# Kernel tuning notes

Measured on AMD Instinct MI355X. Metric: run time of the kernel, lower is better.

The kernel has to match this reference:

```python
import jax, jax.numpy as jnp
import numpy as np

B, T, F = 4096, 60, 30
H, HD, LAT = 256, 100, 256
ACQ_VOCAB = [(50, 16), (10, 8), (5, 4)]
SEQ_VOCAB = [(30, 8), (12, 4), (31, 4)]
DIN = F + 28 + 16  # 74 = seq_n_features + emb_acq_sum + emb_seq_sum
EPS = 1e-5


def setup_inputs() -> dict:
    key = jax.random.key(0)
    ks = iter(jax.random.split(key, 64))

    def nrm(shape, s=0.05):
        return jax.random.normal(next(ks), shape, jnp.float32) * s

    inp = {}
    inp["seq"] = jax.random.normal(next(ks), (B, T, F), jnp.float32)
    inp["seq_len"] = jnp.sort(jax.random.randint(next(ks), (B,), 1, T + 1))[::-1]  # descending (pack_padded)
    inp["ymd"] = jnp.stack([jax.random.randint(next(ks), (B, T), 0, c) for c, _ in SEQ_VOCAB], axis=-1)
    inp["acq"] = jnp.stack([jax.random.randint(next(ks), (B,), 0, c) for c, _ in ACQ_VOCAB], axis=-1)
    inp["macro_pred"] = jax.random.normal(next(ks), (B, 12, 14), jnp.float32)
    inp["z_noise"] = jax.random.normal(next(ks), (B, LAT), jnp.float32)  # reparam noise, fixed for determinism
    for i, (c, d) in enumerate(ACQ_VOCAB):
        inp[f"E_acq{i}"] = nrm((c, d), 1.0)
    for i, (c, d) in enumerate(SEQ_VOCAB):
        inp[f"E_seq{i}"] = nrm((c, d), 1.0)
    for tag in ("f", "b"):  # bidirectional LSTM, 1 layer
        inp[f"Wih_{tag}"] = nrm((4 * H, DIN))
        inp[f"Whh_{tag}"] = nrm((4 * H, H))
        inp[f"bih_{tag}"] = nrm((4 * H,))
        inp[f"bhh_{tag}"] = nrm((4 * H,))
    inp["W_lat"] = nrm((2 * LAT, H)); inp["b_lat"] = nrm((2 * LAT,))
    inp["Wih1"] = nrm((4 * HD, LAT + 9 + 14)); inp["Whh1"] = nrm((4 * HD, HD))
    inp["bih1"] = nrm((4 * HD,)); inp["bhh1"] = nrm((4 * HD,))
    inp["Wih2"] = nrm((4 * HD, HD)); inp["Whh2"] = nrm((4 * HD, HD))
    inp["bih2"] = nrm((4 * HD,)); inp["bhh2"] = nrm((4 * HD,))
    inp["Wg1"] = nrm((25, HD)); inp["bg1"] = nrm((25,))
    inp["gamma"] = jnp.ones((25,), jnp.float32); inp["beta"] = jnp.zeros((25,), jnp.float32)
    inp["Wg2"] = nrm((9, 25)); inp["bg2"] = nrm((9,))
    return inp


def _lstm_cell(x, h, c, Wih, Whh, bih, bhh):
    g = x @ Wih.T + h @ Whh.T + (bih + bhh)
    i, f, gg, o = jnp.split(g, 4, axis=-1)  # torch gate order i,f,g,o
    c = jax.nn.sigmoid(f) * c + jax.nn.sigmoid(i) * jnp.tanh(gg)
    h = jax.nn.sigmoid(o) * jnp.tanh(c)
    return h, c


def _masked_lstm(xs_tm, lens, Wih, Whh, bih, bhh):
    """xs_tm: [T,B,D] time-major. Returns hidden at each sequence's final valid step."""
    h0 = jnp.zeros((xs_tm.shape[1], Whh.shape[1]), xs_tm.dtype)

    def step(carry, inp):
        h, c = carry
        x, t = inp
        hn, cn = _lstm_cell(x, h, c, Wih, Whh, bih, bhh)
        m = (t < lens)[:, None]
        return (jnp.where(m, hn, h), jnp.where(m, cn, c)), None

    (h, _), _ = jax.lax.scan(step, (h0, h0), (xs_tm, jnp.arange(xs_tm.shape[0])))
    return h


def reference(seq, seq_len, ymd, acq, macro_pred, z_noise,
              E_acq0, E_acq1, E_acq2, E_seq0, E_seq1, E_seq2,
              Wih_f, Whh_f, bih_f, bhh_f, Wih_b, Whh_b, bih_b, bhh_b,
              W_lat, b_lat, Wih1, Whh1, bih1, bhh1, Wih2, Whh2, bih2, bhh2,
              Wg1, bg1, gamma, beta, Wg2, bg2):
    Bn, Tn = seq.shape[0], seq.shape[1]
    ea = jnp.concatenate([E_acq0[acq[:, 0]], E_acq1[acq[:, 1]], E_acq2[acq[:, 2]]], axis=1)
    ea = jnp.broadcast_to(ea[:, None, :], (Bn, Tn, ea.shape[1]))
    ey = jnp.concatenate([E_seq0[ymd[:, :, 0]], E_seq1[ymd[:, :, 1]], E_seq2[ymd[:, :, 2]]], axis=2)
    s = jnp.concatenate([seq, ea, ey], axis=2)  # [B,T,74]

    # bidirectional LSTM over valid lengths (pack_padded semantics)
    h_f = _masked_lstm(jnp.swapaxes(s, 0, 1), seq_len, Wih_f, Whh_f, bih_f, bhh_f)
    idx = jnp.clip(seq_len[:, None] - 1 - jnp.arange(Tn)[None, :], 0, Tn - 1)  # per-seq reversed valid indices
    s_rev = jnp.take_along_axis(s, idx[:, :, None], axis=1)
    h_b = _masked_lstm(jnp.swapaxes(s_rev, 0, 1), seq_len, Wih_b, Whh_b, bih_b, bhh_b)

    lat = (h_f + h_b) @ W_lat.T + b_lat  # [B, 2*LAT]
    mu_z, logv = lat[:, :LAT], lat[:, LAT:]
    z = mu_z + jnp.sqrt(jnp.exp(logv)) * z_noise

    dlq0 = jnp.take_along_axis(seq, (seq_len - 1)[:, None, None], axis=1)[:, 0, -9:]  # [B,9]
    h0 = jnp.zeros((Bn, HD), seq.dtype)

    def dec_step(carry, mp_t):
        h1, c1, h2, c2, dlq = carry
        decinp = jnp.concatenate([z, dlq, mp_t], axis=1)  # [B, LAT+9+14]
        h1, c1 = _lstm_cell(decinp, h1, c1, Wih1, Whh1, bih1, bhh1)
        h2, c2 = _lstm_cell(h1, h2, c2, Wih2, Whh2, bih2, bhh2)  # dropout = identity (eval)
        x = jax.nn.relu(h2 @ Wg1.T + bg1)
        mu = x.mean(axis=0)
        var = ((x - mu) ** 2).mean(axis=0)  # train-mode BN, biased var
        x = gamma * (x - mu) * jax.lax.rsqrt(var + EPS) + beta
        dlq = x @ Wg2.T + bg2
        return (h1, c1, h2, c2, dlq), dlq

    _, outs = jax.lax.scan(dec_step, (h0, h0, h0, h0, dlq0), jnp.swapaxes(macro_pred, 0, 1))
    return jnp.transpose(outs, (1, 2, 0))  # [B, 9, 12] (torch.stack(out, 2))
```

## Files before the change

kernel.cpp:

```cpp
#include <hip/hip_runtime.h>
#include <math.h>

#define B_SZ   4096
#define T_SZ   60
#define F_SZ   30
#define H_ENC  256
#define HD_DEC 100
#define LATD   256
#define KM     352
#define KMP    360
#define NKK    11
#define DEC_IN 279
#define DTAIL  24

enum {
  OFF_PWM_F = 0,
  OFF_PWM_B = OFF_PWM_F + 180224,
  OFF_BEN_F = OFF_PWM_B + 180224,
  OFF_BEN_B = OFF_BEN_F + 1024,
  OFF_PLAT  = OFF_BEN_B + 1024,
  OFF_P1I   = OFF_PLAT + 256*256*2,
  OFF_P1H   = OFF_P1I + 280*100*4,
  OFF_P2I   = OFF_P1H + 100*100*4,
  OFF_P2H   = OFF_P2I + 100*100*4,
  OFF_WG1T  = OFF_P2H + 100*100*4,
  OFF_BE1   = OFF_WG1T + 100*25,
  OFF_BE2   = OFF_BE1 + 400,
  OFF_HF    = OFF_BE2 + 400,
  OFF_HB    = OFF_HF + B_SZ*H_ENC,
  OFF_Z     = OFF_HB + B_SZ*H_ENC,
  OFF_H1    = OFF_Z + B_SZ*LATD,
  OFF_C1    = OFF_H1 + B_SZ*HD_DEC,
  OFF_H2    = OFF_C1 + B_SZ*HD_DEC,
  OFF_C2    = OFF_H2 + B_SZ*HD_DEC,
  OFF_DLQ   = OFF_C2 + B_SZ*HD_DEC,
  OFF_XBUF  = OFF_DLQ + B_SZ*9,
  OFF_MU    = OFF_XBUF + B_SZ*25,
  OFF_RSTD  = OFF_MU + 25,
  OFF_ZW1   = OFF_RSTD + 25,
  WS_FLOATS = OFF_ZW1 + B_SZ*400
};

typedef __attribute__((ext_vector_type(8))) short short8v;
typedef __attribute__((ext_vector_type(4))) float f32x4;

__device__ __forceinline__ float sigf(float x) { return 1.0f / (1.0f + expf(-x)); }

__device__ __forceinline__ unsigned short f2bf(float f) {
  union { float f; unsigned int u; } v; v.f = f;
  unsigned int u = v.u + 0x7fffu + ((v.u >> 16) & 1u);
  return (unsigned short)(u >> 16);
}
__device__ __forceinline__ float bf2f(unsigned short s) {
  union { unsigned int u; float f; } v; v.u = ((unsigned int)s) << 16;
  return v.f;
}

struct PJob { const float* a; const float* b; float* dst; int p0, p1, p2, p3, mode; };
struct PrepArgs { PJob j[12]; };

__device__ __forceinline__ float enc_wv(const float* wih, const float* whh, int k, int u, int g) {
  if (k < 74)  return wih[(g * 256 + u) * 74 + k];
  if (k < 76)  return 0.0f;
  if (k < 332) return whh[(g * 256 + u) * 256 + (k - 76)];
  return 0.0f;
}

__global__ __launch_bounds__(256) void prep_kernel(PrepArgs pa) {
  int gtid = blockIdx.x * blockDim.x + threadIdx.x;
  int stride = gridDim.x * blockDim.x;
  for (int jj = 0; jj < 12; ++jj) {
    PJob jb = pa.j[jj];
    if (jb.mode == 1) {
      for (int i = gtid; i < jb.p0; i += stride) jb.dst[i] = jb.a[i] + jb.b[i];
    } else if (jb.mode == 0) {
      int total = jb.p2 * jb.p0;
      for (int i = gtid; i < total; i += stride) {
        int k = i / jb.p0, u = i - k * jb.p0;
        float* d = jb.dst + (size_t)i * jb.p3;
        for (int g = 0; g < jb.p3; ++g)
          d[g] = (k < jb.p1) ? jb.a[(g * jb.p0 + u) * jb.p1 + k] : 0.0f;
      }
    } else if (jb.mode == 4) {
      int total = NKK * 64 * 64;
      for (int i = gtid; i < total; i += stride) {
        int kk = i / 4096, rem = i - kk * 4096;
        int ntg = rem >> 6, l = rem & 63;
        int n = ntg * 16 + (l & 15);
        int u = n >> 2, g = n & 3;
        int kb = kk * 32 + (l >> 4) * 8;
        unsigned int* d = (unsigned int*)jb.dst + (size_t)i * 4;
        for (int wd = 0; wd < 4; ++wd) {
          float lo = enc_wv(jb.a, jb.b, kb + 2 * wd,     u, g);
          float hi = enc_wv(jb.a, jb.b, kb + 2 * wd + 1, u, g);
          d[wd] = (unsigned int)f2bf(lo) | ((unsigned int)f2bf(hi) << 16);
        }
      }
    } else {
      for (int i = gtid; i < 1024; i += stride) {
        int u = i >> 2, g = i & 3;
        jb.dst[i] = jb.a[g * 256 + u] + jb.b[g * 256 + u];
      }
    }
  }
}

#define GDOT(acc, c, w0, w1, w2, w3, xv) \
  acc = fmaf((w0).c, (xv).x, fmaf((w1).c, (xv).y, fmaf((w2).c, (xv).z, fmaf((w3).c, (xv).w, acc))))

__global__ __launch_bounds__(512) void enc_kernel(
    const float* __restrict__ seq, const int* __restrict__ seq_len,
    const int* __restrict__ ymd, const int* __restrict__ acq,
    const float* __restrict__ Ea0, const float* __restrict__ Ea1, const float* __restrict__ Ea2,
    const float* __restrict__ Es0, const float* __restrict__ Es1, const float* __restrict__ Es2,
    const unsigned short* __restrict__ PWMf, const unsigned short* __restrict__ PWMb,
    const float* __restrict__ benF, const float* __restrict__ benB,
    float* __restrict__ hf_out, float* __restrict__ hb_out)
{
  const int tid = threadIdx.x;
  const bool bwd = blockIdx.x >= 128;
  const int c = blockIdx.x & 127;
  const unsigned short* __restrict__ PWM = bwd ? PWMb : PWMf;
  const float* __restrict__ ben = bwd ? benB : benF;
  float* __restrict__ hout = bwd ? hb_out : hf_out;

  __shared__ __align__(16) unsigned short v_s[32][KMP];
  __shared__ float c_s[32][256];
  __shared__ int   len_s[32];

  for (int i = tid; i < 32 * KMP; i += 512) (&v_s[0][0])[i] = 0;
  for (int i = tid; i < 32 * 256; i += 512) (&c_s[0][0])[i] = 0.0f;
  if (tid < 32) len_s[tid] = seq_len[c + 128 * tid];
  __syncthreads();

  for (int i = tid; i < 32 * 28; i += 512) {
    int r = i / 28, d = i - r * 28;
    const int* aq = &acq[(c + 128 * r) * 3];
    float v;
    if (d < 16)      v = Ea0[aq[0] * 16 + d];
    else if (d < 24) v = Ea1[aq[1] * 8 + (d - 16)];
    else             v = Ea2[aq[2] * 4 + (d - 24)];
    v_s[r][30 + d] = f2bf(v);
  }

  const int w   = tid >> 6;
  const int l   = tid & 63;
  const int col = l & 15;
  const int qk  = l >> 4;
  const int g   = l & 3;
  const int usub = col >> 2;

  float bias_r[8];
  #pragma unroll
  for (int nt = 0; nt < 8; ++nt) bias_r[nt] = ben[128 * w + 16 * nt + col];

  __syncthreads();
  const int maxlen = len_s[0];

  for (int t = 0; t < maxlen; ++t) {
    for (int i = tid; i < 1472; i += 512) {
      if (i < 960) {
        int r = i / 30, k = i - r * 30;
        int len = len_s[r];
        int te = bwd ? max(len - 1 - t, 0) : t;
        v_s[r][k] = f2bf(seq[((size_t)(c + 128 * r) * T_SZ + te) * F_SZ + k]);
      } else {
        int ii = i - 960;
        int r = ii >> 4, d = ii & 15;
        int len = len_s[r];
        int te = bwd ? max(len - 1 - t, 0) : t;
        const int* ym = &ymd[((size_t)(c + 128 * r) * T_SZ + te) * 3];
        float v;
        if (d < 8)       v = Es0[ym[0] * 8 + d];
        else if (d < 12) v = Es1[ym[1] * 4 + (d - 8)];
        else             v = Es2[ym[2] * 4 + (d - 12)];
        v_s[r][58 + d] = f2bf(v);
      }
    }
    __syncthreads();

    f32x4 acc0[8], acc1[8];
    #pragma unroll
    for (int nt = 0; nt < 8; ++nt) {
      acc0[nt][0] = bias_r[nt]; acc0[nt][1] = bias_r[nt];
      acc0[nt][2] = bias_r[nt]; acc0[nt][3] = bias_r[nt];
      acc1[nt] = acc0[nt];
    }

    for (int kk = 0; kk < NKK; ++kk) {
      short8v a0 = *reinterpret_cast<const short8v*>(&v_s[col][32 * kk + 8 * qk]);
      short8v a1 = *reinterpret_cast<const short8v*>(&v_s[16 + col][32 * kk + 8 * qk]);
      const unsigned short* Bk = PWM + ((size_t)kk * 4096 + l) * 8;
      #pragma unroll
      for (int nt = 0; nt < 8; ++nt) {
        int ntg = 8 * w + nt;
        short8v b = *reinterpret_cast<const short8v*>(Bk + (size_t)ntg * 512);
        acc0[nt] = __builtin_amdgcn_mfma_f32_16x16x32_bf16(a0, b, acc0[nt], 0, 0, 0);
        acc1[nt] = __builtin_amdgcn_mfma_f32_16x16x32_bf16(a1, b, acc1[nt], 0, 0, 0);
      }
    }
    __syncthreads();

    #pragma unroll
    for (int rt = 0; rt < 2; ++rt) {
      #pragma unroll
      for (int nt = 0; nt < 8; ++nt) {
        int u = 32 * w + 4 * nt + usub;
        #pragma unroll
        for (int i = 0; i < 4; ++i) {
          int row = 16 * rt + qk * 4 + i;
          float val = rt == 0 ? acc0[nt][i] : acc1[nt][i];
          float act = (g == 2) ? tanhf(val) : sigf(val);
          float a1s = __shfl_xor(act, 1);
          float a2s = __shfl_xor(act, 2);
          float a3s = __shfl_xor(a1s, 2);
          if (g == 0 && t < len_s[row]) {
            float cc = c_s[row][u];
            float cn = a1s * cc + act * a2s;
            c_s[row][u] = cn;
            v_s[row][76 + u] = f2bf(a3s * tanhf(cn));
          }
        }
      }
    }
  }

  __syncthreads();
  for (int i = tid; i < 32 * 256; i += 512) {
    int r = i >> 8, u = i & 255;
    hout[(size_t)(c + 128 * r) * H_ENC + u] = bf2f(v_s[r][76 + u]);
  }
}

__global__ __launch_bounds__(256) void latent_kernel(
    const float* __restrict__ hf, const float* __restrict__ hb,
    const float2* __restrict__ Plat, const float* __restrict__ b_lat,
    const float* __restrict__ z_noise, const float* __restrict__ seq,
    const int* __restrict__ seq_len,
    float* __restrict__ z, float* __restrict__ dlq,
    float* __restrict__ h1w, float* __restrict__ c1w,
    float* __restrict__ h2w, float* __restrict__ c2w)
{
  const int tid = threadIdx.x;
  const int b0 = blockIdx.x * 16;
  __shared__ float hs[16][H_ENC];
  for (int i = tid; i < 16 * H_ENC; i += 256)
    (&hs[0][0])[i] = hf[b0 * H_ENC + i] + hb[b0 * H_ENC + i];
  __syncthreads();

  const int u = tid;
  const float bm = b_lat[u], bv = b_lat[LATD + u];
  float am[16], av[16];
  #pragma unroll
  for (int r = 0; r < 16; ++r) { am[r] = bm; av[r] = bv; }

  for (int k = 0; k < H_ENC; k += 4) {
    const float2 p0 = Plat[(k + 0) * 256 + u];
    const float2 p1 = Plat[(k + 1) * 256 + u];
    const float2 p2 = Plat[(k + 2) * 256 + u];
    const float2 p3 = Plat[(k + 3) * 256 + u];
    #pragma unroll
    for (int r = 0; r < 16; ++r) {
      const float4 hv = *reinterpret_cast<const float4*>(&hs[r][k]);
      am[r] = fmaf(p0.x, hv.x, fmaf(p1.x, hv.y, fmaf(p2.x, hv.z, fmaf(p3.x, hv.w, am[r]))));
      av[r] = fmaf(p0.y, hv.x, fmaf(p1.y, hv.y, fmaf(p2.y, hv.z, fmaf(p3.y, hv.w, av[r]))));
    }
  }
  #pragma unroll
  for (int r = 0; r < 16; ++r) {
    int b = b0 + r;
    z[b * LATD + u] = am[r] + sqrtf(expf(av[r])) * z_noise[b * LATD + u];
  }
  if (u < HD_DEC) {
    #pragma unroll
    for (int r = 0; r < 16; ++r) {
      int b = b0 + r;
      h1w[b * HD_DEC + u] = 0.0f; c1w[b * HD_DEC + u] = 0.0f;
      h2w[b * HD_DEC + u] = 0.0f; c2w[b * HD_DEC + u] = 0.0f;
    }
  }
  if (u < 9) {
    #pragma unroll
    for (int r = 0; r < 16; ++r) {
      int b = b0 + r;
      int len = seq_len[b];
      dlq[b * 9 + u] = seq[(b * T_SZ + (len - 1)) * F_SZ + 21 + u];
    }
  }
}

__global__ __launch_bounds__(256) void dec_zpre_kernel(
    const float* __restrict__ z, const float4* __restrict__ P1I,
    float* __restrict__ zw1)
{
  const int tid = threadIdx.x;
  const int b0 = blockIdx.x * 16;
  __shared__ float zs[16][LATD];
  for (int i = tid; i < 16 * LATD; i += 256)
    (&zs[0][0])[i] = z[b0 * LATD + i];
  __syncthreads();

  const int u = tid & 127;
  const int grp = tid >> 7;
  const int r0 = grp * 8;
  if (u >= HD_DEC) return;

  float a0[8], a1[8], a2[8], a3[8];
  #pragma unroll
  for (int r = 0; r < 8; ++r) { a0[r] = 0.0f; a1[r] = 0.0f; a2[r] = 0.0f; a3[r] = 0.0f; }
  for (int k = 0; k < LATD; k += 4) {
    const float4 w0 = P1I[(k + 0) * 100 + u];
    const float4 w1 = P1I[(k + 1) * 100 + u];
    const float4 w2 = P1I[(k + 2) * 100 + u];
    const float4 w3 = P1I[(k + 3) * 100 + u];
    #pragma unroll
    for (int r = 0; r < 8; ++r) {
      const float4 xv = *reinterpret_cast<const float4*>(&zs[r0 + r][k]);
      GDOT(a0[r], x, w0, w1, w2, w3, xv);
      GDOT(a1[r], y, w0, w1, w2, w3, xv);
      GDOT(a2[r], z, w0, w1, w2, w3, xv);
      GDOT(a3[r], w, w0, w1, w2, w3, xv);
    }
  }
  #pragma unroll
  for (int r = 0; r < 8; ++r) {
    int b = b0 + r0 + r;
    zw1[b * 400 + u]       = a0[r];
    zw1[b * 400 + 100 + u] = a1[r];
    zw1[b * 400 + 200 + u] = a2[r];
    zw1[b * 400 + 300 + u] = a3[r];
  }
}

__global__ __launch_bounds__(256) void dec_cell_kernel(
    const float* __restrict__ zw1, const float* __restrict__ dlq,
    const float* __restrict__ macro,
    float* __restrict__ h1w, float* __restrict__ c1w,
    float* __restrict__ h2w, float* __restrict__ c2w,
    const float4* __restrict__ P1I, const float4* __restrict__ P1H, const float* __restrict__ be1,
    const float4* __restrict__ P2I, const float4* __restrict__ P2H, const float* __restrict__ be2,
    const float* __restrict__ Wg1T, const float* __restrict__ bg1,
    float* __restrict__ xbuf, int t)
{
  const int tid = threadIdx.x;
  const int b0 = blockIdx.x * 16;
  __shared__ float di[16][DTAIL];
  __shared__ float h1s[16][HD_DEC];
  __shared__ float h2s[16][HD_DEC];

  for (int i = tid; i < 16 * DTAIL; i += 256) {
    int r = i / DTAIL, k = i - r * DTAIL;
    int b = b0 + r;
    float v;
    if (k < 9)       v = dlq[b * 9 + k];
    else if (k < 23) v = macro[(b * 12 + t) * 14 + (k - 9)];
    else             v = 0.0f;
    di[r][k] = v;
  }
  for (int i = tid; i < 16 * HD_DEC; i += 256) {
    int r = i / HD_DEC, k = i - r * HD_DEC;
    h1s[r][k] = h1w[(b0 + r) * HD_DEC + k];
    h2s[r][k] = h2w[(b0 + r) * HD_DEC + k];
  }

  const int u = tid & 127;
  const int grp = tid >> 7;
  const int r0 = grp * 8;
  const bool act = u < HD_DEC;

  float c1r[8], c2r[8];
  if (act) {
    #pragma unroll
    for (int r = 0; r < 8; ++r) {
      c1r[r] = c1w[(b0 + r0 + r) * HD_DEC + u];
      c2r[r] = c2w[(b0 + r0 + r) * HD_DEC + u];
    }
  }
  __syncthreads();

  float a0[8], a1[8], a2[8], a3[8];
  if (act) {
    const float b0g = be1[u], b1g = be1[100 + u], b2g = be1[200 + u], b3g = be1[300 + u];
    #pragma unroll
    for (int r = 0; r < 8; ++r) {
      const float* zw = &zw1[(size_t)(b0 + r0 + r) * 400];
      a0[r] = b0g + zw[u];
      a1[r] = b1g + zw[100 + u];
      a2[r] = b2g + zw[200 + u];
      a3[r] = b3g + zw[300 + u];
    }
    for (int k = 0; k < DTAIL; k += 4) {
      const int kk = LATD + k;
      const float4 w0 = P1I[(kk + 0) * 100 + u];
      const float4 w1 = P1I[(kk + 1) * 100 + u];
      const float4 w2 = P1I[(kk + 2) * 100 + u];
      const float4 w3 = P1I[(kk + 3) * 100 + u];
      #pragma unroll
      for (int r = 0; r < 8; ++r) {
        const float4 xv = *reinterpret_cast<const float4*>(&di[r0 + r][k]);
        GDOT(a0[r], x, w0, w1, w2, w3, xv);
        GDOT(a1[r], y, w0, w1, w2, w3, xv);
        GDOT(a2[r], z, w0, w1, w2, w3, xv);
        GDOT(a3[r], w, w0, w1, w2, w3, xv);
      }
    }
    for (int k = 0; k < HD_DEC; k += 4) {
      const float4 w0 = P1H[(k + 0) * 100 + u];
      const float4 w1 = P1H[(k + 1) * 100 + u];
      const float4 w2 = P1H[(k + 2) * 100 + u];
      const float4 w3 = P1H[(k + 3) * 100 + u];
      #pragma unroll
      for (int r = 0; r < 8; ++r) {
        const float4 hv = *reinterpret_cast<const float4*>(&h1s[r0 + r][k]);
        GDOT(a0[r], x, w0, w1, w2, w3, hv);
        GDOT(a1[r], y, w0, w1, w2, w3, hv);
        GDOT(a2[r], z, w0, w1, w2, w3, hv);
        GDOT(a3[r], w, w0, w1, w2, w3, hv);
      }
    }
  }
  __syncthreads();
  if (act) {
    #pragma unroll
    for (int r = 0; r < 8; ++r) {
      float ig = sigf(a0[r]), fg = sigf(a1[r]), gg = tanhf(a2[r]), og = sigf(a3[r]);
      float cn = fg * c1r[r] + ig * gg;
      float hn = og * tanhf(cn);
      int b = b0 + r0 + r;
      h1s[r0 + r][u] = hn;
      h1w[b * HD_DEC + u] = hn;
      c1w[b * HD_DEC + u] = cn;
    }
  }
  __syncthreads();

  if (act) {
    const float b0g = be2[u], b1g = be2[100 + u], b2g = be2[200 + u], b3g = be2[300 + u];
    #pragma unroll
    for (int r = 0; r < 8; ++r) { a0[r] = b0g; a1[r] = b1g; a2[r] = b2g; a3[r] = b3g; }
    for (int k = 0; k < HD_DEC; k += 4) {
      const float4 w0 = P2I[(k + 0) * 100 + u];
      const float4 w1 = P2I[(k + 1) * 100 + u];
      const float4 w2 = P2I[(k + 2) * 100 + u];
      const float4 w3 = P2I[(k + 3) * 100 + u];
      #pragma unroll
      for (int r = 0; r < 8; ++r) {
        const float4 hv = *reinterpret_cast<const float4*>(&h1s[r0 + r][k]);
        GDOT(a0[r], x, w0, w1, w2, w3, hv);
        GDOT(a1[r], y, w0, w1, w2, w3, hv);
        GDOT(a2[r], z, w0, w1, w2, w3, hv);
        GDOT(a3[r], w, w0, w1, w2, w3, hv);
      }
    }
    for (int k = 0; k < HD_DEC; k += 4) {
      const float4 w0 = P2H[(k + 0) * 100 + u];
      const float4 w1 = P2H[(k + 1) * 100 + u];
      const float4 w2 = P2H[(k + 2) * 100 + u];
      const float4 w3 = P2H[(k + 3) * 100 + u];
      #pragma unroll
      for (int r = 0; r < 8; ++r) {
        const float4 hv = *reinterpret_cast<const float4*>(&h2s[r0 + r][k]);
        GDOT(a0[r], x, w0, w1, w2, w3, hv);
        GDOT(a1[r], y, w0, w1, w2, w3, hv);
        GDOT(a2[r], z, w0, w1, w2, w3, hv);
        GDOT(a3[r], w, w0, w1, w2, w3, hv);
      }
    }
  }
  __syncthreads();
  if (act) {
    #pragma unroll
    for (int r = 0; r < 8; ++r) {
      float ig = sigf(a0[r]), fg = sigf(a1[r]), gg = tanhf(a2[r]), og = sigf(a3[r]);
      float cn = fg * c2r[r] + ig * gg;
      float hn = og * tanhf(cn);
      int b = b0 + r0 + r;
      h2s[r0 + r][u] = hn;
      h2w[b * HD_DEC + u] = hn;
      c2w[b * HD_DEC + u] = cn;
    }
  }
  __syncthreads();

  for (int p = tid; p < 16 * 25; p += 256) {
    int r = p / 25, cc = p - r * 25;
    float s = bg1[cc];
    for (int k = 0; k < HD_DEC; k += 4) {
      const float4 hv = *reinterpret_cast<const float4*>(&h2s[r][k]);
      s += hv.x * Wg1T[k * 25 + cc] + hv.y * Wg1T[(k + 1) * 25 + cc]
         + hv.z * Wg1T[(k + 2) * 25 + cc] + hv.w * Wg1T[(k + 3) * 25 + cc];
    }
    xbuf[(b0 + r) * 25 + cc] = fmaxf(s, 0.0f);
  }
}

__global__ __launch_bounds__(256) void dec_stats_kernel(
    const float* __restrict__ xbuf, float* __restrict__ muv, float* __restrict__ rstdv)
{
  const int col = blockIdx.x;
  const int tid = threadIdx.x;
  __shared__ float red[256];
  float v[16];
  float s = 0.0f;
  #pragma unroll
  for (int i = 0; i < 16; ++i) { v[i] = xbuf[(tid + 256 * i) * 25 + col]; s += v[i]; }
  red[tid] = s; __syncthreads();
  for (int off = 128; off >= 1; off >>= 1) {
    if (tid < off) red[tid] += red[tid + off];
    __syncthreads();
  }
  float mean = red[0] / (float)B_SZ;
  __syncthreads();
  float s2 = 0.0f;
  #pragma unroll
  for (int i = 0; i < 16; ++i) { float d = v[i] - mean; s2 += d * d; }
  red[tid] = s2; __syncthreads();
  for (int off = 128; off >= 1; off >>= 1) {
    if (tid < off) red[tid] += red[tid + off];
    __syncthreads();
  }
  if (tid == 0) {
    muv[col] = mean;
    rstdv[col] = rsqrtf(red[0] / (float)B_SZ + 1e-5f);
  }
}

__global__ __launch_bounds__(256) void dec_out_kernel(
    const float* __restrict__ xbuf, const float* __restrict__ muv, const float* __restrict__ rstdv,
    const float* __restrict__ gamma, const float* __restrict__ beta,
    const float* __restrict__ Wg2, const float* __restrict__ bg2,
    float* __restrict__ dlq, float* __restrict__ out, int t)
{
  int b = blockIdx.x * 256 + threadIdx.x;
  float xn[25];
  #pragma unroll
  for (int c = 0; c < 25; ++c)
    xn[c] = gamma[c] * (xbuf[b * 25 + c] - muv[c]) * rstdv[c] + beta[c];
  #pragma unroll
  for (int j = 0; j < 9; ++j) {
    float s = bg2[j];
    #pragma unroll
    for (int c = 0; c < 25; ++c) s += xn[c] * Wg2[j * 25 + c];
    dlq[b * 9 + j] = s;
    out[b * 108 + j * 12 + t] = s;
  }
}

extern "C" void kernel_launch(void* const* d_in, const int* in_sizes, int n_in,
                              void* d_out, int out_size, void* d_ws, size_t ws_size,
                              hipStream_t stream)
{
  const float* seq     = (const float*)d_in[0];
  const int*   seq_len = (const int*)  d_in[1];
  const int*   ymd     = (const int*)  d_in[2];
  const int*   acq     = (const int*)  d_in[3];
  const float* macro   = (const float*)d_in[4];
  const float* z_noise = (const float*)d_in[5];
  const float* Ea0 = (const float*)d_in[6];
  const float* Ea1 = (const float*)d_in[7];
  const float* Ea2 = (const float*)d_in[8];
  const float* Es0 = (const float*)d_in[9];
  const float* Es1 = (const float*)d_in[10];
  const float* Es2 = (const float*)d_in[11];
  const float* Wih_f = (const float*)d_in[12];
  const float* Whh_f = (const float*)d_in[13];
  const float* bih_f = (const float*)d_in[14];
  const float* bhh_f = (const float*)d_in[15];
  const float* Wih_b = (const float*)d_in[16];
  const float* Whh_b = (const float*)d_in[17];
  const float* bih_b = (const float*)d_in[18];
  const float* bhh_b = (const float*)d_in[19];
  const float* W_lat = (const float*)d_in[20];
  const float* b_lat = (const float*)d_in[21];
  const float* Wih1  = (const float*)d_in[22];
  const float* Whh1  = (const float*)d_in[23];
  const float* bih1  = (const float*)d_in[24];
  const float* bhh1  = (const float*)d_in[25];
  const float* Wih2  = (const float*)d_in[26];
  const float* Whh2  = (const float*)d_in[27];
  const float* bih2  = (const float*)d_in[28];
  const float* bhh2  = (const float*)d_in[29];
  const float* Wg1   = (const float*)d_in[30];
  const float* bg1   = (const float*)d_in[31];
  const float* gamma = (const float*)d_in[32];
  const float* beta  = (const float*)d_in[33];
  const float* Wg2   = (const float*)d_in[34];
  const float* bg2   = (const float*)d_in[35];

  float* ws  = (float*)d_ws;
  float* out = (float*)d_out;

  float* pwmF = ws + OFF_PWM_F;
  float* pwmB = ws + OFF_PWM_B;
  float* benF = ws + OFF_BEN_F;
  float* benB = ws + OFF_BEN_B;
  float* plat = ws + OFF_PLAT;
  float* p1i  = ws + OFF_P1I;
  float* p1h  = ws + OFF_P1H;
  float* p2i  = ws + OFF_P2I;
  float* p2h  = ws + OFF_P2H;
  float* wg1T = ws + OFF_WG1T;
  float* be1  = ws + OFF_BE1;
  float* be2  = ws + OFF_BE2;
  float* hf   = ws + OFF_HF;
  float* hb   = ws + OFF_HB;
  float* z    = ws + OFF_Z;
  float* h1w  = ws + OFF_H1;
  float* c1w  = ws + OFF_C1;
  float* h2w  = ws + OFF_H2;
  float* c2w  = ws + OFF_C2;
  float* dlq  = ws + OFF_DLQ;
  float* xbuf = ws + OFF_XBUF;
  float* muv  = ws + OFF_MU;
  float* rstdv= ws + OFF_RSTD;
  float* zw1  = ws + OFF_ZW1;

  PrepArgs pa;
  int ji = 0;
  auto JOB = [&](const float* a, const float* b, float* d, int p0, int p1, int p2, int p3, int m) {
    pa.j[ji].a = a; pa.j[ji].b = b; pa.j[ji].dst = d;
    pa.j[ji].p0 = p0; pa.j[ji].p1 = p1; pa.j[ji].p2 = p2; pa.j[ji].p3 = p3; pa.j[ji].mode = m; ++ji;
  };
  JOB(Wih_f, Whh_f, pwmF, 0,0,0,0, 4);
  JOB(Wih_b, Whh_b, pwmB, 0,0,0,0, 4);
  JOB(bih_f, bhh_f, benF, 0,0,0,0, 5);
  JOB(bih_b, bhh_b, benB, 0,0,0,0, 5);
  JOB(W_lat, nullptr, plat, 256, 256, 256, 2, 0);
  JOB(Wih1,  nullptr, p1i,  100, 279, 280, 4, 0);
  JOB(Whh1,  nullptr, p1h,  100, 100, 100, 4, 0);
  JOB(Wih2,  nullptr, p2i,  100, 100, 100, 4, 0);
  JOB(Whh2,  nullptr, p2h,  100, 100, 100, 4, 0);
  JOB(Wg1,   nullptr, wg1T, 25, 100, 100, 1, 0);
  JOB(bih1,  bhh1,  be1,  400, 0,0,0, 1);
  JOB(bih2,  bhh2,  be2,  400, 0,0,0, 1);

  prep_kernel<<<512, 256, 0, stream>>>(pa);

  enc_kernel<<<256, 512, 0, stream>>>(
      seq, seq_len, ymd, acq, Ea0, Ea1, Ea2, Es0, Es1, Es2,
      (const unsigned short*)pwmF, (const unsigned short*)pwmB,
      benF, benB, hf, hb);

  latent_kernel<<<256, 256, 0, stream>>>(
      hf, hb, (const float2*)plat, b_lat, z_noise, seq, seq_len,
      z, dlq, h1w, c1w, h2w, c2w);

  dec_zpre_kernel<<<256, 256, 0, stream>>>(z, (const float4*)p1i, zw1);

  for (int t = 0; t < 12; ++t) {
    dec_cell_kernel<<<256, 256, 0, stream>>>(
        zw1, dlq, macro, h1w, c1w, h2w, c2w,
        (const float4*)p1i, (const float4*)p1h, be1,
        (const float4*)p2i, (const float4*)p2h, be2, wg1T, bg1, xbuf, t);
    dec_stats_kernel<<<25, 256, 0, stream>>>(xbuf, muv, rstdv);
    dec_out_kernel<<<16, 256, 0, stream>>>(
        xbuf, muv, rstdv, gamma, beta, Wg2, bg2, dlq, out, t);
  }
}
```

Measured before the change: 3.108 ms.

## Fuse z-projection into latent kernel and BN output into next decoder cell

```diff
diff --git a/kernel.cpp b/kernel.cpp
--- a/kernel.cpp
+++ b/kernel.cpp
@@ -10,7 +10,6 @@
 #define KM     352
 #define KMP    360
 #define NKK    11
-#define DEC_IN 279
 #define DTAIL  24
 
 enum {
@@ -28,8 +27,7 @@
   OFF_BE2   = OFF_BE1 + 400,
   OFF_HF    = OFF_BE2 + 400,
   OFF_HB    = OFF_HF + B_SZ*H_ENC,
-  OFF_Z     = OFF_HB + B_SZ*H_ENC,
-  OFF_H1    = OFF_Z + B_SZ*LATD,
+  OFF_H1    = OFF_HB + B_SZ*H_ENC,
   OFF_C1    = OFF_H1 + B_SZ*HD_DEC,
   OFF_H2    = OFF_C1 + B_SZ*HD_DEC,
   OFF_C2    = OFF_H2 + B_SZ*HD_DEC,
@@ -236,8 +234,8 @@
     const float* __restrict__ hf, const float* __restrict__ hb,
     const float2* __restrict__ Plat, const float* __restrict__ b_lat,
     const float* __restrict__ z_noise, const float* __restrict__ seq,
-    const int* __restrict__ seq_len,
-    float* __restrict__ z, float* __restrict__ dlq,
+    const int* __restrict__ seq_len, const float4* __restrict__ P1I,
+    float* __restrict__ dlq, float* __restrict__ zw1,
     float* __restrict__ h1w, float* __restrict__ c1w,
     float* __restrict__ h2w, float* __restrict__ c2w)
 {
@@ -266,11 +264,6 @@
       av[r] = fmaf(p0.y, hv.x, fmaf(p1.y, hv.y, fmaf(p2.y, hv.z, fmaf(p3.y, hv.w, av[r]))));
     }
   }
-  #pragma unroll
-  for (int r = 0; r < 16; ++r) {
-    int b = b0 + r;
-    z[b * LATD + u] = am[r] + sqrtf(expf(av[r])) * z_noise[b * LATD + u];
-  }
   if (u < HD_DEC) {
     #pragma unroll
     for (int r = 0; r < 16; ++r) {
@@ -287,80 +280,96 @@
       dlq[b * 9 + u] = seq[(b * T_SZ + (len - 1)) * F_SZ + 21 + u];
     }
   }
-}
-
-__global__ __launch_bounds__(256) void dec_zpre_kernel(
-    const float* __restrict__ z, const float4* __restrict__ P1I,
-    float* __restrict__ zw1)
-{
-  const int tid = threadIdx.x;
-  const int b0 = blockIdx.x * 16;
-  __shared__ float zs[16][LATD];
-  for (int i = tid; i < 16 * LATD; i += 256)
-    (&zs[0][0])[i] = z[b0 * LATD + i];
-  __syncthreads();
-
-  const int u = tid & 127;
+  __syncthreads();
+  #pragma unroll
+  for (int r = 0; r < 16; ++r) {
+    int b = b0 + r;
+    hs[r][u] = am[r] + sqrtf(expf(av[r])) * z_noise[b * LATD + u];
+  }
+  __syncthreads();
+
+  const int uu = tid & 127;
   const int grp = tid >> 7;
   const int r0 = grp * 8;
-  if (u >= HD_DEC) return;
-
-  float a0[8], a1[8], a2[8], a3[8];
-  #pragma unroll
-  for (int r = 0; r < 8; ++r) { a0[r] = 0.0f; a1[r] = 0.0f; a2[r] = 0.0f; a3[r] = 0.0f; }
-  for (int k = 0; k < LATD; k += 4) {
-    const float4 w0 = P1I[(k + 0) * 100 + u];
-    const float4 w1 = P1I[(k + 1) * 100 + u];
-    const float4 w2 = P1I[(k + 2) * 100 + u];
-    const float4 w3 = P1I[(k + 3) * 100 + u];
+  if (uu < HD_DEC) {
+    float a0[8], a1[8], a2[8], a3[8];
+    #pragma unroll
+    for (int r = 0; r < 8; ++r) { a0[r] = 0.0f; a1[r] = 0.0f; a2[r] = 0.0f; a3[r] = 0.0f; }
+    for (int k = 0; k < LATD; k += 4) {
+      const float4 w0 = P1I[(k + 0) * 100 + uu];
+      const float4 w1 = P1I[(k + 1) * 100 + uu];
+      const float4 w2 = P1I[(k + 2) * 100 + uu];
+      const float4 w3 = P1I[(k + 3) * 100 + uu];
+      #pragma unroll
+      for (int r = 0; r < 8; ++r) {
+        const float4 xv = *reinterpret_cast<const float4*>(&hs[r0 + r][k]);
+        GDOT(a0[r], x, w0, w1, w2, w3, xv);
+        GDOT(a1[r], y, w0, w1, w2, w3, xv);
+        GDOT(a2[r], z, w0, w1, w2, w3, xv);
+        GDOT(a3[r], w, w0, w1, w2, w3, xv);
+      }
+    }
     #pragma unroll
     for (int r = 0; r < 8; ++r) {
-      const float4 xv = *reinterpret_cast<const float4*>(&zs[r0 + r][k]);
-      GDOT(a0[r], x, w0, w1, w2, w3, xv);
-      GDOT(a1[r], y, w0, w1, w2, w3, xv);
-      GDOT(a2[r], z, w0, w1, w2, w3, xv);
-      GDOT(a3[r], w, w0, w1, w2, w3, xv);
-    }
-  }
-  #pragma unroll
-  for (int r = 0; r < 8; ++r) {
-    int b = b0 + r0 + r;
-    zw1[b * 400 + u]       = a0[r];
-    zw1[b * 400 + 100 + u] = a1[r];
-    zw1[b * 400 + 200 + u] = a2[r];
-    zw1[b * 400 + 300 + u] = a3[r];
+      int b = b0 + r0 + r;
+      zw1[b * 400 + uu]       = a0[r];
+      zw1[b * 400 + 100 + uu] = a1[r];
+      zw1[b * 400 + 200 + uu] = a2[r];
+      zw1[b * 400 + 300 + uu] = a3[r];
+    }
   }
 }
 
 __global__ __launch_bounds__(256) void dec_cell_kernel(
-    const float* __restrict__ zw1, const float* __restrict__ dlq,
+    const float* __restrict__ zw1, const float* __restrict__ dlq0,
     const float* __restrict__ macro,
     float* __restrict__ h1w, float* __restrict__ c1w,
     float* __restrict__ h2w, float* __restrict__ c2w,
     const float4* __restrict__ P1I, const float4* __restrict__ P1H, const float* __restrict__ be1,
     const float4* __restrict__ P2I, const float4* __restrict__ P2H, const float* __restrict__ be2,
     const float* __restrict__ Wg1T, const float* __restrict__ bg1,
-    float* __restrict__ xbuf, int t)
+    const float* __restrict__ muv, const float* __restrict__ rstdv,
+    const float* __restrict__ gamma, const float* __restrict__ beta,
+    const float* __restrict__ Wg2, const float* __restrict__ bg2,
+    float* __restrict__ xbuf, float* __restrict__ out, int t)
 {
   const int tid = threadIdx.x;
   const int b0 = blockIdx.x * 16;
   __shared__ float di[16][DTAIL];
+  __shared__ float xns[16][25];
   __shared__ float h1s[16][HD_DEC];
   __shared__ float h2s[16][HD_DEC];
 
-  for (int i = tid; i < 16 * DTAIL; i += 256) {
-    int r = i / DTAIL, k = i - r * DTAIL;
-    int b = b0 + r;
-    float v;
-    if (k < 9)       v = dlq[b * 9 + k];
-    else if (k < 23) v = macro[(b * 12 + t) * 14 + (k - 9)];
-    else             v = 0.0f;
-    di[r][k] = v;
+  if (t > 0) {
+    for (int p = tid; p < 16 * 25; p += 256) {
+      int r = p / 25, cc = p - r * 25;
+      xns[r][cc] = gamma[cc] * (xbuf[(b0 + r) * 25 + cc] - muv[cc]) * rstdv[cc] + beta[cc];
+    }
+  } else {
+    for (int p = tid; p < 16 * 9; p += 256) {
+      int r = p / 9, j = p - r * 9;
+      di[r][j] = dlq0[(b0 + r) * 9 + j];
+    }
+  }
+  for (int i = tid; i < 16 * 15; i += 256) {
+    int r = i / 15, k = i - r * 15;
+    di[r][9 + k] = (k < 14) ? macro[((size_t)(b0 + r) * 12 + t) * 14 + k] : 0.0f;
   }
   for (int i = tid; i < 16 * HD_DEC; i += 256) {
     int r = i / HD_DEC, k = i - r * HD_DEC;
     h1s[r][k] = h1w[(b0 + r) * HD_DEC + k];
     h2s[r][k] = h2w[(b0 + r) * HD_DEC + k];
+  }
+  __syncthreads();
+  if (t > 0) {
+    for (int p = tid; p < 16 * 9; p += 256) {
+      int r = p / 9, j = p - r * 9;
+      float s = bg2[j];
+      #pragma unroll
+      for (int cc = 0; cc < 25; ++cc) s += xns[r][cc] * Wg2[j * 25 + cc];
+      di[r][j] = s;
+      out[(size_t)(b0 + r) * 108 + j * 12 + (t - 1)] = s;
+    }
   }
 
   const int u = tid & 127;
@@ -525,11 +534,11 @@
   }
 }
 
-__global__ __launch_bounds__(256) void dec_out_kernel(
+__global__ __launch_bounds__(256) void dec_finalout_kernel(
     const float* __restrict__ xbuf, const float* __restrict__ muv, const float* __restrict__ rstdv,
     const float* __restrict__ gamma, const float* __restrict__ beta,
     const float* __restrict__ Wg2, const float* __restrict__ bg2,
-    float* __restrict__ dlq, float* __restrict__ out, int t)
+    float* __restrict__ out)
 {
   int b = blockIdx.x * 256 + threadIdx.x;
   float xn[25];
@@ -541,8 +550,7 @@
     float s = bg2[j];
     #pragma unroll
     for (int c = 0; c < 25; ++c) s += xn[c] * Wg2[j * 25 + c];
-    dlq[b * 9 + j] = s;
-    out[b * 108 + j * 12 + t] = s;
+    out[(size_t)b * 108 + j * 12 + 11] = s;
   }
 }
 
@@ -604,7 +612,6 @@
   float* be2  = ws + OFF_BE2;
   float* hf   = ws + OFF_HF;
   float* hb   = ws + OFF_HB;
-  float* z    = ws + OFF_Z;
   float* h1w  = ws + OFF_H1;
   float* c1w  = ws + OFF_C1;
   float* h2w  = ws + OFF_H2;
@@ -643,17 +650,16 @@
 
   latent_kernel<<<256, 256, 0, stream>>>(
       hf, hb, (const float2*)plat, b_lat, z_noise, seq, seq_len,
-      z, dlq, h1w, c1w, h2w, c2w);
-
-  dec_zpre_kernel<<<256, 256, 0, stream>>>(z, (const float4*)p1i, zw1);
+      (const float4*)p1i, dlq, zw1, h1w, c1w, h2w, c2w);
 
   for (int t = 0; t < 12; ++t) {
     dec_cell_kernel<<<256, 256, 0, stream>>>(
         zw1, dlq, macro, h1w, c1w, h2w, c2w,
         (const float4*)p1i, (const float4*)p1h, be1,
-        (const float4*)p2i, (const float4*)p2h, be2, wg1T, bg1, xbuf, t);
+        (const float4*)p2i, (const float4*)p2h, be2, wg1T, bg1,
+        muv, rstdv, gamma, beta, Wg2, bg2, xbuf, out, t);
     dec_stats_kernel<<<25, 256, 0, stream>>>(xbuf, muv, rstdv);
-    dec_out_kernel<<<16, 256, 0, stream>>>(
-        xbuf, muv, rstdv, gamma, beta, Wg2, bg2, dlq, out, t);
-  }
-}
+  }
+  dec_finalout_kernel<<<16, 256, 0, stream>>>(
+      xbuf, muv, rstdv, gamma, beta, Wg2, bg2, out);
+}
```

Measured after the change: 3.020 ms (median of 2 runs). -2.8%, faster.
